# Performance work log

Hardware: AMD Instinct MI355X
Metric: run time of the kernel (lower is better)

The kernel has to match this reference:

```python
import jax, jax.numpy as jnp
import numpy as np

F, D = 4, 64          # n_facet, emb_dim
FD = F * D            # cur_dim = 256
NITER = 3             # args.iter

def _embed(x, W, b):
    # SparseInputLinear: torch.mm(x, weight) + bias
    return x @ W + b

def _homo(self_e, neigh_e, a):
    # HomoAttention(emb_dim, n_facet): per-facet gated fusion of self and neighbor embeds
    B = self_e.shape[0]
    s = self_e.reshape(B, F, D)
    n = neigh_e.reshape(B, F, D)
    score = jax.nn.leaky_relu(jnp.concatenate([s, n], axis=-1) @ a, 0.2)  # [B,F]
    alpha = jax.nn.sigmoid(score)[..., None]
    return (s + alpha * n).reshape(B, FD)

def _norm(x):
    return x / (jnp.linalg.norm(x, axis=-1, keepdims=True) + 1e-8)

def _hete(self_e, stacked):
    # HeteAttention(emb_dim, n_facet, niter): disentangled routing over K relation channels
    B, K = stacked.shape[0], stacked.shape[1]
    u0 = _norm(self_e.reshape(B, F, D))
    z = _norm(stacked.reshape(B, K, F, D))
    u = u0
    for _ in range(NITER):
        p = jax.nn.softmax(jnp.einsum('bfd,bkfd->bkf', u, z), axis=1)
        u = _norm(u0 + jnp.einsum('bkf,bkfd->bfd', p, z))
    return u.reshape(B, FD)

def setup_inputs() -> dict:
    key = jax.random.key(0)
    ks = jax.random.split(key, 32)
    B, NU, NB, NC, NG = 1024, 20000, 20000, 1000, 500
    def r(i, shape):
        return jax.random.uniform(ks[i], shape, dtype=jnp.float32)
    def p(i, shape, fan):
        s = 1.0 / np.sqrt(fan)
        return jax.random.uniform(ks[i], shape, minval=-s, maxval=s, dtype=jnp.float32)
    return {
        "users": r(0, (B, NU)), "businesses": r(1, (B, NB)),
        "u_neigh_user": r(2, (B, NU)), "u_neigh_business": r(3, (B, NB)),
        "u_neigh_city": r(4, (B, NC)), "u_neigh_category": r(5, (B, NG)),
        "b_neigh_user": r(6, (B, NU)), "b_neigh_business": r(7, (B, NB)),
        "b_neigh_city": r(8, (B, NC)), "b_neigh_category": r(9, (B, NG)),
        "W_user": p(10, (NU, FD), FD), "b_user": p(11, (FD,), FD),
        "W_bus": p(12, (NB, FD), FD), "b_bus": p(13, (FD,), FD),
        "W_city": p(14, (NC, FD), FD), "b_city": p(15, (FD,), FD),
        "W_cat": p(16, (NG, FD), FD), "b_cat": p(17, (FD,), FD),
        "homo_a": p(18, (8, 2 * D), 2 * D),
    }

def reference(users, businesses, u_neigh_user, u_neigh_business, u_neigh_city, u_neigh_category,
              b_neigh_user, b_neigh_business, b_neigh_city, b_neigh_category,
              W_user, b_user, W_bus, b_bus, W_city, b_city, W_cat, b_cat, homo_a):
    user_embed = _embed(users, W_user, b_user)
    business_embed = _embed(businesses, W_bus, b_bus)
    Ws = [(W_user, b_user), (W_bus, b_bus), (W_city, b_city), (W_cat, b_cat)]
    u_neighs = [u_neigh_user, u_neigh_business, u_neigh_city, u_neigh_category]
    b_neighs = [b_neigh_user, b_neigh_business, b_neigh_city, b_neigh_category]
    u_list = [_homo(user_embed, _embed(n, W, b), homo_a[i])
              for i, (n, (W, b)) in enumerate(zip(u_neighs, Ws))]
    updated_user = _hete(user_embed, jnp.stack(u_list, axis=1))
    b_list = [_homo(business_embed, _embed(n, W, b), homo_a[4 + i])
              for i, (n, (W, b)) in enumerate(zip(b_neighs, Ws))]
    # NOTE: original torch code passes user_embed (not business_embed) as the self
    # node to the business hete encoder; we reproduce that faithfully.
    updated_business = _hete(user_embed, jnp.stack(b_list, axis=1))
    # UserItemAttention / autocross: per-facet interaction logits, softmax over dim=1
    logit = jnp.einsum('bfd,bfd->bf',
                       updated_user.reshape(-1, F, D),
                       updated_business.reshape(-1, F, D))
    return jax.nn.softmax(logit, axis=1)
```

## Files before the change

kernel.cpp:

```cpp
#include <hip/hip_runtime.h>
#include <hip/hip_bf16.h>
#include <stdint.h>
#include <stddef.h>

typedef __attribute__((ext_vector_type(8))) _Float16 f16x8;
typedef __attribute__((ext_vector_type(4))) float f32x4;

#define B_ROWS 1024
#define ND 256

struct ConvArgs {
  const float* W[4];
  unsigned short* dst[4];
  int K[4];
  int chBase[4];
};

__global__ void conv_w_kernel(ConvArgs a){
  int cb = blockIdx.x;
  int w = 0;
  if (cb >= a.chBase[1]) w = 1;
  if (cb >= a.chBase[2]) w = 2;
  if (cb >= a.chBase[3]) w = 3;
  int c = cb - a.chBase[w];
  __shared__ float tile[32][257];
  const float* Wp = a.W[w];
  int K = a.K[w];
  int t = threadIdx.x;
  const float* src = Wp + (size_t)c * 32 * ND;
  bool full = (c * 32 + 32 <= K);
  #pragma unroll
  for (int j = 0; j < 8; ++j){
    int idx = j * 256 + t;
    int row = idx >> 6;
    int col = (idx & 63) * 4;
    float4 v;
    if (full || (c * 32 + row < K)) v = *(const float4*)(src + (size_t)idx * 4);
    else { v.x = v.y = v.z = v.w = 0.f; }
    tile[row][col+0] = v.x; tile[row][col+1] = v.y;
    tile[row][col+2] = v.z; tile[row][col+3] = v.w;
  }
  __syncthreads();
  int n = t;
  union { unsigned short s[32]; uint4 v[4]; } pk;
  #pragma unroll
  for (int k = 0; k < 32; ++k){
    _Float16 h = (_Float16)tile[k][n];
    pk.s[k] = *(unsigned short*)&h;
  }
  unsigned short* d = a.dst[w] + ((size_t)c * ND + n) * 32;
  #pragma unroll
  for (int q = 0; q < 4; ++q) *(uint4*)(d + q*8) = pk.v[q];
}

struct BiasArgs { float* emb; const float* b[10]; };

__global__ void bias_init_kernel(BiasArgs a){
  int idx = blockIdx.x * blockDim.x + threadIdx.x;
  int g  = idx >> 16;
  int wi = idx & 65535;
  int n4 = (wi & 63) * 4;
  const float* bp = a.b[g];
  float4 v; v.x = bp[n4]; v.y = bp[n4+1]; v.z = bp[n4+2]; v.w = bp[n4+3];
  *(float4*)(a.emb + (size_t)idx * 4) = v;
}

struct GemmArgs {
  const float* X[10];
  const unsigned short* Wh[10];
  float* C[10];
  int K[10];
  int nch[10];
  int ksplit[10];
  int wgBase[11];
};

__launch_bounds__(256, 4)
__global__ void gemm_kernel(GemmArgs a){
  __shared__ _Float16 Ahi[2][64][32];
  __shared__ _Float16 Alo[2][64][32];

  int nx = (int)gridDim.x >> 3;
  int bid = ((int)blockIdx.x & 7) * nx + ((int)blockIdx.x >> 3);

  int g = 0;
  while (bid >= a.wgBase[g+1]) ++g;
  int loc = bid - a.wgBase[g];
  int mt = loc & 15;
  int ks = loc >> 4;
  int nch = a.nch[g], ksp = a.ksplit[g];
  int q = nch / ksp, r = nch % ksp;
  int c0  = ks * q + (ks < r ? ks : r);
  int cnt = q + (ks < r ? 1 : 0);

  const float* X = a.X[g];
  int K = a.K[g];
  const unsigned short* Wh = a.Wh[g];

  int t = threadIdx.x;
  int lane = t & 63, w = t >> 6;
  int ln15 = lane & 15, kg = lane >> 4;
  int rowbase = mt * 64;

  int srow = t >> 2, skg = t & 3;
  const float* xsrc = X + (size_t)(rowbase + srow) * K + skg * 8;

  f32x4 acc[4][4];
  #pragma unroll
  for (int i = 0; i < 4; ++i)
    #pragma unroll
    for (int j = 0; j < 4; ++j) acc[i][j] = (f32x4){0.f,0.f,0.f,0.f};

  auto ldA = [&](float* d, int c){
    int k0 = c * 32 + skg * 8;
    if (k0 + 8 <= K){
      float4 v0 = *(const float4*)(xsrc + c*32);
      float4 v1 = *(const float4*)(xsrc + c*32 + 4);
      d[0]=v0.x; d[1]=v0.y; d[2]=v0.z; d[3]=v0.w;
      d[4]=v1.x; d[5]=v1.y; d[6]=v1.z; d[7]=v1.w;
    } else {
      for (int j = 0; j < 8; ++j) d[j] = (k0 + j < K) ? xsrc[c*32 + j] : 0.f;
    }
  };
  auto stA = [&](int buf, const float* v){
    _Float16 hh[8], ll[8];
    #pragma unroll
    for (int j = 0; j < 8; ++j){
      _Float16 h = (_Float16)v[j];
      hh[j] = h;
      ll[j] = (_Float16)(v[j] - (float)h);
    }
    *(f16x8*)&Ahi[buf][srow][skg*8] = *(f16x8*)hh;
    *(f16x8*)&Alo[buf][srow][skg*8] = *(f16x8*)ll;
  };

  {
    float v[8];
    ldA(v, c0);
    stA(0, v);
  }

  for (int ci = 0; ci < cnt; ++ci){
    int c = c0 + ci;
    int cur = ci & 1;
    __syncthreads();
    f16x8 bh[4];
    size_t cb = (size_t)c * (ND * 32);
    #pragma unroll
    for (int j = 0; j < 4; ++j)
      bh[j] = *(const f16x8*)(Wh + cb + (size_t)(w*64 + j*16 + ln15) * 32 + kg*8);
    float v[8];
    bool pre = (ci + 1 < cnt);
    if (pre) ldA(v, c + 1);
    #pragma unroll
    for (int i = 0; i < 4; ++i){
      f16x8 ah = *(const f16x8*)&Ahi[cur][i*16 + ln15][kg*8];
      f16x8 al = *(const f16x8*)&Alo[cur][i*16 + ln15][kg*8];
      #pragma unroll
      for (int j = 0; j < 4; ++j){
        acc[i][j] = __builtin_amdgcn_mfma_f32_16x16x32_f16(ah, bh[j], acc[i][j], 0, 0, 0);
        acc[i][j] = __builtin_amdgcn_mfma_f32_16x16x32_f16(al, bh[j], acc[i][j], 0, 0, 0);
      }
    }
    if (pre) stA(cur ^ 1, v);
  }

  float* C = a.C[g];
  int crow0 = kg * 4;
  #pragma unroll
  for (int i = 0; i < 4; ++i){
    #pragma unroll
    for (int j = 0; j < 4; ++j){
      int col = w*64 + j*16 + ln15;
      #pragma unroll
      for (int rr = 0; rr < 4; ++rr){
        int row = rowbase + i*16 + crow0 + rr;
        atomicAdd(&C[(size_t)row * ND + col], acc[i][j][rr]);
      }
    }
  }
}

__device__ __forceinline__ float wsum(float v){
  #pragma unroll
  for (int m = 32; m; m >>= 1) v += __shfl_xor(v, m, 64);
  return v;
}

__global__ void fuse_kernel(const float* __restrict__ emb,
                            const float* __restrict__ homo_a,
                            float* __restrict__ out){
  int b = blockIdx.x;
  int t = threadIdx.x;
  int f = t >> 6;
  int d = t & 63;
  auto E = [&](int g){ return emb[((size_t)g * B_ROWS + b) * ND + t]; };

  float us = E(0), bs = E(1);
  float un[4], bn[4];
  #pragma unroll
  for (int i = 0; i < 4; ++i){ un[i] = E(2+i); bn[i] = E(6+i); }

  float ul[4], blv[4];
  #pragma unroll
  for (int i = 0; i < 4; ++i){
    float as_ = homo_a[i*128 + d],     an_ = homo_a[i*128 + 64 + d];
    float sc  = wsum(us*as_ + un[i]*an_);
    sc = sc > 0.f ? sc : 0.2f*sc;
    float alp = 1.f / (1.f + expf(-sc));
    ul[i] = us + alp*un[i];
    float as2 = homo_a[(4+i)*128 + d], an2 = homo_a[(4+i)*128 + 64 + d];
    float sc2 = wsum(bs*as2 + bn[i]*an2);
    sc2 = sc2 > 0.f ? sc2 : 0.2f*sc2;
    float alp2 = 1.f / (1.f + expf(-sc2));
    blv[i] = bs + alp2*bn[i];
  }

  float u0 = us / (sqrtf(wsum(us*us)) + 1e-8f);
  float zu[4], zb[4];
  #pragma unroll
  for (int i = 0; i < 4; ++i){
    zu[i] = ul[i]  / (sqrtf(wsum(ul[i]*ul[i]))   + 1e-8f);
    zb[i] = blv[i] / (sqrtf(wsum(blv[i]*blv[i])) + 1e-8f);
  }

  auto route = [&](float z0, float z1, float z2, float z3)->float{
    float u = u0;
    #pragma unroll
    for (int it = 0; it < 3; ++it){
      float d0 = wsum(u*z0), d1 = wsum(u*z1), d2 = wsum(u*z2), d3 = wsum(u*z3);
      float m = fmaxf(fmaxf(d0,d1), fmaxf(d2,d3));
      float e0 = expf(d0-m), e1 = expf(d1-m), e2 = expf(d2-m), e3 = expf(d3-m);
      float s = e0+e1+e2+e3;
      float nu = u0 + (e0*z0 + e1*z1 + e2*z2 + e3*z3) / s;
      u = nu / (sqrtf(wsum(nu*nu)) + 1e-8f);
    }
    return u;
  };

  float uu = route(zu[0], zu[1], zu[2], zu[3]);
  float ub = route(zb[0], zb[1], zb[2], zb[3]);

  float lg = wsum(uu*ub);
  __shared__ float sl[4];
  if (d == 0) sl[f] = lg;
  __syncthreads();
  if (t < 4){
    float l0 = sl[0], l1 = sl[1], l2 = sl[2], l3 = sl[3];
    float m = fmaxf(fmaxf(l0,l1), fmaxf(l2,l3));
    float den = expf(l0-m) + expf(l1-m) + expf(l2-m) + expf(l3-m);
    out[(size_t)b*4 + t] = expf(sl[t]-m) / den;
  }
}

extern "C" void kernel_launch(void* const* d_in, const int* in_sizes, int n_in,
                              void* d_out, int out_size, void* d_ws, size_t ws_size,
                              hipStream_t stream) {
  const float* X[10];
  for (int i = 0; i < 10; ++i) X[i] = (const float*)d_in[i];
  const float* Wm[4]   = { (const float*)d_in[10], (const float*)d_in[12],
                           (const float*)d_in[14], (const float*)d_in[16] };
  const float* bias[4] = { (const float*)d_in[11], (const float*)d_in[13],
                           (const float*)d_in[15], (const float*)d_in[17] };
  const float* homo_a  = (const float*)d_in[18];
  float* out = (float*)d_out;

  const size_t EMB_FLOATS = 10ull * B_ROWS * ND;
  float* emb = (float*)d_ws;
  unsigned short* wch = (unsigned short*)((char*)d_ws + EMB_FLOATS * 4);
  const int nchW[4] = {625, 625, 32, 16};
  const int Kw[4]   = {20000, 20000, 1000, 500};
  size_t off[4];
  {
    size_t o = 0;
    for (int w = 0; w < 4; ++w){ off[w] = o; o += (size_t)nchW[w] * ND * 32; }
  }

  ConvArgs ca;
  int cbase = 0;
  for (int w = 0; w < 4; ++w){
    ca.W[w] = Wm[w];
    ca.dst[w] = wch + off[w];
    ca.K[w] = Kw[w];
    ca.chBase[w] = cbase;
    cbase += nchW[w];
  }
  hipLaunchKernelGGL(conv_w_kernel, dim3(cbase), dim3(256), 0, stream, ca);

  static const int biasOf[10] = {0,1,0,1,2,3,0,1,2,3};
  BiasArgs ba;
  ba.emb = emb;
  for (int g = 0; g < 10; ++g) ba.b[g] = bias[biasOf[g]];
  hipLaunchKernelGGL(bias_init_kernel, dim3((EMB_FLOATS/4)/256), dim3(256), 0, stream, ba);

  static const int wOf[10] = {0,1,0,1,2,3,0,1,2,3};
  static const int ksp[10] = {7,7,7,7,2,1,7,7,2,1};
  GemmArgs ga;
  int base = 0;
  for (int g = 0; g < 10; ++g){
    ga.X[g]  = X[g];
    ga.Wh[g] = wch + off[wOf[g]];
    ga.C[g]  = emb + (size_t)g * B_ROWS * ND;
    ga.K[g]  = Kw[wOf[g]];
    ga.nch[g] = nchW[wOf[g]];
    ga.ksplit[g] = ksp[g];
    ga.wgBase[g] = base;
    base += 16 * ksp[g];
  }
  ga.wgBase[10] = base;
  hipLaunchKernelGGL(gemm_kernel, dim3(base), dim3(256), 0, stream, ga);

  hipLaunchKernelGGL(fuse_kernel, dim3(B_ROWS), dim3(256), 0, stream, emb, homo_a, out);
}
```

Baseline: 561.8 us.

## Deepen GEMM prefetch pipeline, remap LDS layout, and raise split-K

Restructures the split-fp16 GEMM main loop so the A tile is prefetched two chunks ahead and B one chunk ahead in registers, overlapping more global latency with MFMA work. The A shared-memory buffers are remapped into a lane-indexed f16x8 layout so each wave reads its fragment contiguously, which avoids bank conflicts. The split-K factor for the large 20000-wide GEMMs rises from 7 to 16, adding workgroups and parallelism at the cost of more atomicAdd traffic. Launch bounds drop to 3 waves per SIMD to make room for the extra registers.

```diff
diff --git a/kernel.cpp b/kernel.cpp
--- a/kernel.cpp
+++ b/kernel.cpp
@@ -75,10 +75,9 @@
   int wgBase[11];
 };
 
-__launch_bounds__(256, 4)
+__launch_bounds__(256, 3)
 __global__ void gemm_kernel(GemmArgs a){
-  __shared__ _Float16 Ahi[2][64][32];
-  __shared__ _Float16 Alo[2][64][32];
+  __shared__ f16x8 Abuf[2][2][4][64];
 
   int nx = (int)gridDim.x >> 3;
   int bid = ((int)blockIdx.x & 7) * nx + ((int)blockIdx.x >> 3);
@@ -103,6 +102,7 @@
   int rowbase = mt * 64;
 
   int srow = t >> 2, skg = t & 3;
+  int wslot = (lane & 3) * 16 + (lane >> 2);
   const float* xsrc = X + (size_t)(rowbase + srow) * K + skg * 8;
 
   f32x4 acc[4][4];
@@ -130,39 +130,49 @@
       hh[j] = h;
       ll[j] = (_Float16)(v[j] - (float)h);
     }
-    *(f16x8*)&Ahi[buf][srow][skg*8] = *(f16x8*)hh;
-    *(f16x8*)&Alo[buf][srow][skg*8] = *(f16x8*)ll;
+    Abuf[buf][0][w][wslot] = *(f16x8*)hh;
+    Abuf[buf][1][w][wslot] = *(f16x8*)ll;
   };
-
+  auto ldB = [&](f16x8* b, int c){
+    size_t cb = (size_t)c * (ND * 32);
+    #pragma unroll
+    for (int j = 0; j < 4; ++j)
+      b[j] = *(const f16x8*)(Wh + cb + (size_t)(w*64 + j*16 + ln15) * 32 + kg*8);
+  };
+
+  float r1[8], r2[8];
+  f16x8 bcur[4], bnxt[4];
   {
-    float v[8];
-    ldA(v, c0);
-    stA(0, v);
+    float v0[8];
+    ldA(v0, c0);
+    stA(0, v0);
+    ldB(bcur, c0);
+    if (cnt > 1) ldA(r1, c0 + 1);
   }
 
   for (int ci = 0; ci < cnt; ++ci){
     int c = c0 + ci;
     int cur = ci & 1;
     __syncthreads();
-    f16x8 bh[4];
-    size_t cb = (size_t)c * (ND * 32);
-    #pragma unroll
-    for (int j = 0; j < 4; ++j)
-      bh[j] = *(const f16x8*)(Wh + cb + (size_t)(w*64 + j*16 + ln15) * 32 + kg*8);
-    float v[8];
-    bool pre = (ci + 1 < cnt);
-    if (pre) ldA(v, c + 1);
+    bool pre1 = (ci + 1 < cnt);
+    bool pre2 = (ci + 2 < cnt);
+    if (pre1) ldB(bnxt, c + 1);
+    if (pre2) ldA(r2, c + 2);
     #pragma unroll
     for (int i = 0; i < 4; ++i){
-      f16x8 ah = *(const f16x8*)&Ahi[cur][i*16 + ln15][kg*8];
-      f16x8 al = *(const f16x8*)&Alo[cur][i*16 + ln15][kg*8];
+      f16x8 ah = Abuf[cur][0][i][lane];
+      f16x8 al = Abuf[cur][1][i][lane];
       #pragma unroll
       for (int j = 0; j < 4; ++j){
-        acc[i][j] = __builtin_amdgcn_mfma_f32_16x16x32_f16(ah, bh[j], acc[i][j], 0, 0, 0);
-        acc[i][j] = __builtin_amdgcn_mfma_f32_16x16x32_f16(al, bh[j], acc[i][j], 0, 0, 0);
+        acc[i][j] = __builtin_amdgcn_mfma_f32_16x16x32_f16(ah, bcur[j], acc[i][j], 0, 0, 0);
+        acc[i][j] = __builtin_amdgcn_mfma_f32_16x16x32_f16(al, bcur[j], acc[i][j], 0, 0, 0);
       }
     }
-    if (pre) stA(cur ^ 1, v);
+    if (pre1) stA(cur ^ 1, r1);
+    #pragma unroll
+    for (int j = 0; j < 8; ++j) r1[j] = r2[j];
+    #pragma unroll
+    for (int j = 0; j < 4; ++j) bcur[j] = bnxt[j];
   }
 
   float* C = a.C[g];
@@ -294,7 +304,7 @@
   hipLaunchKernelGGL(bias_init_kernel, dim3((EMB_FLOATS/4)/256), dim3(256), 0, stream, ba);
 
   static const int wOf[10] = {0,1,0,1,2,3,0,1,2,3};
-  static const int ksp[10] = {7,7,7,7,2,1,7,7,2,1};
+  static const int ksp[10] = {16,16,16,16,2,1,16,16,2,1};
   GemmArgs ga;
   int base = 0;
   for (int g = 0; g < 10; ++g){
```

Result: slower. 620.2 us (+10.4%).
